# Optimization experiments

Measured on AMD Instinct MI355X. Metric: run time of the kernel, lower is better.

The kernel has to match this reference:

```python
import jax, jax.numpy as jnp
import numpy as np

NEG_SLOPE = 0.2
BN_EPS = 1e-5


def gat_conv(x, src, dst, num_nodes, W, att_src, att_dst, bias, concat):
    # x: [N, F_in]; W: [F_in, H*C]; att_src/att_dst: [H, C]
    H, C = att_src.shape
    h = (x @ W).reshape(num_nodes, H, C)                 # [N, H, C]
    a_src = jnp.einsum('nhc,hc->nh', h, att_src)          # [N, H]
    a_dst = jnp.einsum('nhc,hc->nh', h, att_dst)          # [N, H]
    e = a_src[src] + a_dst[dst]                           # [E, H]
    e = jax.nn.leaky_relu(e, NEG_SLOPE)
    # segment softmax over edges sharing the same destination node
    m = jax.ops.segment_max(e, dst, num_segments=num_nodes)   # [N, H]
    ex = jnp.exp(e - m[dst])
    denom = jax.ops.segment_sum(ex, dst, num_segments=num_nodes)  # [N, H]
    alpha = ex / (denom[dst] + 1e-16)                     # [E, H]
    msg = h[src] * alpha[:, :, None]                      # [E, H, C]
    out = jax.ops.segment_sum(msg, dst, num_segments=num_nodes)   # [N, H, C]
    if concat:
        return out.reshape(num_nodes, H * C) + bias
    return out.mean(axis=1) + bias


def batch_norm(x, gamma, beta):
    mu = x.mean(axis=0)
    var = x.var(axis=0)
    return (x - mu) * jax.lax.rsqrt(var + BN_EPS) * gamma + beta


def setup_inputs() -> dict:
    key = jax.random.key(0)
    ks = jax.random.split(key, 16)
    N, E, F_in, C, H, NC = 50000, 800000, 128, 16, 8, 2
    s = lambda k, shape, fan: jax.random.normal(k, shape, jnp.float32) * (1.0 / np.sqrt(fan))
    inp = {
        'x': jax.random.normal(ks[0], (N, F_in), jnp.float32),
        'edge_index': jax.random.randint(ks[1], (2, E), 0, N, jnp.int32),
        'W0': s(ks[2], (F_in, H * C), F_in),
        'att_src0': s(ks[3], (H, C), C),
        'att_dst0': s(ks[4], (H, C), C),
        'b0': jnp.zeros((H * C,), jnp.float32),
        'gamma0': jnp.ones((H * C,), jnp.float32),
        'beta0': jnp.zeros((H * C,), jnp.float32),
        'W1': s(ks[5], (H * C, H * C), H * C),
        'att_src1': s(ks[6], (H, C), C),
        'att_dst1': s(ks[7], (H, C), C),
        'b1': jnp.zeros((C,), jnp.float32),
        'gamma1': jnp.ones((C,), jnp.float32),
        'beta1': jnp.zeros((C,), jnp.float32),
        'Wc': s(ks[8], (C, NC), C),
        'bc': jnp.zeros((NC,), jnp.float32),
    }
    return inp


def reference(x, edge_index, W0, att_src0, att_dst0, b0, gamma0, beta0,
              W1, att_src1, att_dst1, b1, gamma1, beta1, Wc, bc):
    N = x.shape[0]
    loop = jnp.arange(N, dtype=edge_index.dtype)
    src = jnp.concatenate([edge_index[0], loop])  # add self-loops (PyG default)
    dst = jnp.concatenate([edge_index[1], loop])
    # layer 0: concat heads -> [N, H*C]
    h = gat_conv(x, src, dst, N, W0, att_src0, att_dst0, b0, concat=True)
    h = batch_norm(h, gamma0, beta0)
    h = jax.nn.elu(h)
    # layer 1: average heads -> [N, C]
    h = gat_conv(h, src, dst, N, W1, att_src1, att_dst1, b1, concat=False)
    h = batch_norm(h, gamma1, beta1)
    logits = h @ Wc + bc
    return logits
```

## Files before the change

kernel.cpp:

```cpp
#include <hip/hip_runtime.h>
#include <math.h>

#define NEG_SLOPE 0.2f
#define BN_EPS 1e-5f

typedef __attribute__((ext_vector_type(8))) short bf16x8;
typedef __attribute__((ext_vector_type(4))) float f32x4;
typedef __attribute__((ext_vector_type(8))) unsigned short us8;


__device__ __forceinline__ void edge_sd(const int* __restrict__ ei, int E, int eid, int& s, int& d) {
    if (eid < E) { s = ei[eid]; d = ei[E + eid]; }
    else         { s = d = eid - E; }
}

__device__ __forceinline__ float lrelu(float v) { return v > 0.f ? v : NEG_SLOPE * v; }

__device__ __forceinline__ unsigned short f2bf(float f) {
    unsigned u = __float_as_uint(f);
    u += 0x7fffu + ((u >> 16) & 1u);
    return (unsigned short)(u >> 16);
}

__global__ void wtrans_kernel(const float* __restrict__ W0, const float* __restrict__ as0,
                              const float* __restrict__ ad0,
                              const float* __restrict__ W1, const float* __restrict__ as1,
                              const float* __restrict__ ad1,
                              unsigned short* __restrict__ Wt0, unsigned short* __restrict__ Wt1) {
    int idx = blockIdx.x * 256 + threadIdx.x;
    const float *W, *as_, *ad_;
    unsigned short* Wt;
    int i;
    if (idx < 18432) { W = W0; as_ = as0; ad_ = ad0; Wt = Wt0; i = idx; }
    else             { W = W1; as_ = as1; ad_ = ad1; Wt = Wt1; i = idx - 18432; }
    if (i < 16384) {
        int k = i >> 7, n = i & 127;
        Wt[(n >> 4) * 2048 + (n & 15) * 128 + k] = f2bf(W[k * 128 + n]);
    } else {
        int j = i - 16384;
        int k = j >> 4, hh = j & 15;
        int h = hh & 7;
        const float* av = (hh < 8) ? as_ : ad_;
        float s = 0.f;
#pragma unroll
        for (int c = 0; c < 16; c++) s += W[k * 128 + h * 16 + c] * av[h * 16 + c];
        Wt[8 * 2048 + hh * 128 + k] = f2bf(s);
    }
}

__global__ __launch_bounds__(256) void gemm_att_kernel(const float* __restrict__ X,
                                                       const unsigned short* __restrict__ Wt,
                                                       unsigned short* __restrict__ Hbf,
                                                       float* __restrict__ a_src,
                                                       float* __restrict__ a_dst,
                                                       const float* __restrict__ bnmu,
                                                       const float* __restrict__ bnrs,
                                                       const float* __restrict__ gamma,
                                                       const float* __restrict__ beta,
                                                       int Nrows) {
    __shared__ unsigned short xs[64 * 136];
    int bm = blockIdx.x * 64;
    int tid = threadIdx.x;

    for (int i = tid; i < 64 * 16; i += 256) {
        int row = i >> 4;
        int c8 = (i & 15) * 8;
        int grow = bm + row;
        float v[8];
        if (grow < Nrows) {
            float4 v0 = *(const float4*)(X + (size_t)grow * 128 + c8);
            float4 v1 = *(const float4*)(X + (size_t)grow * 128 + c8 + 4);
            v[0] = v0.x; v[1] = v0.y; v[2] = v0.z; v[3] = v0.w;
            v[4] = v1.x; v[5] = v1.y; v[6] = v1.z; v[7] = v1.w;
        } else {
#pragma unroll
            for (int j = 0; j < 8; j++) v[j] = 0.f;
        }
        if (bnmu != nullptr) {
#pragma unroll
            for (int j = 0; j < 8; j++) {
                int c = c8 + j;
                float t = (v[j] - bnmu[c]) * bnrs[c] * gamma[c] + beta[c];
                v[j] = t > 0.f ? t : expm1f(t);
            }
        }
        us8 p;
#pragma unroll
        for (int j = 0; j < 8; j++) p[j] = f2bf(v[j]);
        *(us8*)(xs + row * 136 + c8) = p;
    }
    __syncthreads();

    int w = tid >> 6, lane = tid & 63;
    int m16 = lane & 15;
    int quad = lane >> 4;

    f32x4 acc[9];
#pragma unroll
    for (int c = 0; c < 9; c++) acc[c] = (f32x4){0.f, 0.f, 0.f, 0.f};

    const unsigned short* xrow = xs + (w * 16 + m16) * 136 + quad * 8;
#pragma unroll
    for (int ks = 0; ks < 4; ks++) {
        bf16x8 a = *(const bf16x8*)(xrow + ks * 32);
#pragma unroll
        for (int c = 0; c < 9; c++) {
            bf16x8 b = *(const bf16x8*)(Wt + c * 2048 + m16 * 128 + ks * 32 + quad * 8);
            acc[c] = __builtin_amdgcn_mfma_f32_16x16x32_bf16(a, b, acc[c], 0, 0, 0);
        }
    }

    int rowb = bm + w * 16 + quad * 4;
#pragma unroll
    for (int c = 0; c < 8; c++) {
#pragma unroll
        for (int r = 0; r < 4; r++) {
            int row = rowb + r;
            if (row < Nrows)
                Hbf[(size_t)row * 128 + c * 16 + m16] = f2bf(acc[c][r]);
        }
    }
#pragma unroll
    for (int r = 0; r < 4; r++) {
        int row = rowb + r;
        if (row < Nrows) {
            if (m16 < 8) a_src[row * 8 + m16] = acc[8][r];
            else         a_dst[row * 8 + (m16 - 8)] = acc[8][r];
        }
    }
}

__global__ void hist_kernel(const int* __restrict__ ei, int E, int Etot,
                            int* __restrict__ counts, int* __restrict__ rank) {
    int eid = blockIdx.x * 256 + threadIdx.x;
    if (eid >= Etot) return;
    int s, d;
    edge_sd(ei, E, eid, s, d);
    rank[eid] = atomicAdd(&counts[d], 1);
}

__global__ __launch_bounds__(256) void chunksum_kernel(const int* __restrict__ counts,
                                                       int* __restrict__ csum, int N) {
    __shared__ int red[256];
    int base = blockIdx.x * 1024;
    int s = 0;
    for (int i = threadIdx.x; i < 1024; i += 256) {
        int idx = base + i;
        s += (idx < N) ? counts[idx] : 0;
    }
    red[threadIdx.x] = s;
    __syncthreads();
#pragma unroll
    for (int st = 128; st > 0; st >>= 1) {
        if (threadIdx.x < st) red[threadIdx.x] += red[threadIdx.x + st];
        __syncthreads();
    }
    if (threadIdx.x == 0) csum[blockIdx.x] = red[0];
}

__global__ void chunkscan_kernel(int* __restrict__ csum, int nchunk) {
    int lane = threadIdx.x;
    int v = (lane < nchunk) ? csum[lane] : 0;
    int incl = v;
#pragma unroll
    for (int off = 1; off < 64; off <<= 1) {
        int t = __shfl_up(incl, off);
        if (lane >= off) incl += t;
    }
    if (lane < nchunk) csum[lane] = incl - v;
}

__global__ __launch_bounds__(1024) void scanfinal_kernel(const int* __restrict__ counts,
                                                         const int* __restrict__ csum,
                                                         int* __restrict__ rowptr, int N) {
    __shared__ int wsum[16], woff_s[16];
    int tid = threadIdx.x, lane = tid & 63, wid = tid >> 6;
    int idx = blockIdx.x * 1024 + tid;
    int v = (idx < N) ? counts[idx] : 0;
    int incl = v;
#pragma unroll
    for (int off = 1; off < 64; off <<= 1) {
        int t = __shfl_up(incl, off);
        if (lane >= off) incl += t;
    }
    if (lane == 63) wsum[wid] = incl;
    __syncthreads();
    if (wid == 0 && lane < 16) {
        int w = wsum[lane], iw = w;
#pragma unroll
        for (int off = 1; off < 16; off <<= 1) {
            int t = __shfl_up(iw, off);
            if (lane >= off) iw += t;
        }
        woff_s[lane] = iw - w;
    }
    __syncthreads();
    if (idx < N) rowptr[idx + 1] = csum[blockIdx.x] + woff_s[wid] + incl;
    if (blockIdx.x == 0 && tid == 0) rowptr[0] = 0;
}

__global__ void scatter_kernel(const int* __restrict__ ei, int E, int Etot,
                               const int* __restrict__ rowptr, const int* __restrict__ rank,
                               unsigned short* __restrict__ ssrc) {
    int eid = blockIdx.x * 256 + threadIdx.x;
    if (eid >= Etot) return;
    int s, d;
    edge_sd(ei, E, eid, s, d);
    ssrc[rowptr[d] + rank[eid]] = (unsigned short)s;
}

template <bool MEAN>
__global__ __launch_bounds__(256) void agg_kernel(const int* __restrict__ rowptr,
                                                  const unsigned short* __restrict__ ssrc,
                                                  const float* __restrict__ a_src,
                                                  const float* __restrict__ a_dst,
                                                  const unsigned short* __restrict__ Hbf,
                                                  float* __restrict__ outbuf, int N) {
    int wid = threadIdx.x >> 6;
    int dst = blockIdx.x * 4 + wid;
    if (dst >= N) return;
    int lane = threadIdx.x & 63;
    int j  = lane >> 3;
    int hj = lane & 7;
    int hf = lane >> 3;
    int f  = lane * 2;
    int start = rowptr[dst], end = rowptr[dst + 1];
    float adst = a_dst[dst * 8 + hj];

    float acc0 = 0.f, acc1 = 0.f, denl = 0.f;
    for (int base = start; base < end; base += 8) {
        int i = base + j;
        int s = (i < end) ? (int)ssrc[i] : -1;
        float w = 0.f;
        if (s >= 0) w = __expf(lrelu(a_src[s * 8 + hj] + adst));
        denl += w;

        int   sA[8];
        float wA[8];
        unsigned uA[8];
#pragma unroll
        for (int j2 = 0; j2 < 8; j2++) {
            sA[j2] = __shfl(s, j2 * 8);
            wA[j2] = __shfl(w, j2 * 8 + hf);
        }
#pragma unroll
        for (int j2 = 0; j2 < 8; j2++)
            uA[j2] = (sA[j2] >= 0) ? *(const unsigned*)(Hbf + (size_t)sA[j2] * 128 + f) : 0u;
#pragma unroll
        for (int j2 = 0; j2 < 8; j2++) {
            acc0 += wA[j2] * __uint_as_float(uA[j2] << 16);
            acc1 += wA[j2] * __uint_as_float(uA[j2] & 0xffff0000u);
        }
    }
#pragma unroll
    for (int off = 8; off < 64; off <<= 1) denl += __shfl_xor(denl, off);
    float den = __shfl(denl, hf);
    float inv = 1.f / (den + 1e-16f);
    if (!MEAN) {
        *(float2*)(outbuf + (size_t)dst * 128 + f) = make_float2(acc0 * inv, acc1 * inv);
    } else {
        float r0 = acc0 * inv, r1 = acc1 * inv;
#pragma unroll
        for (int off = 8; off < 64; off <<= 1) {
            r0 += __shfl_xor(r0, off);
            r1 += __shfl_xor(r1, off);
        }
        if (lane < 8)
            *(float2*)(outbuf + (size_t)dst * 16 + lane * 2) =
                make_float2(r0 * 0.125f, r1 * 0.125f);
    }
}

template <int C>
__global__ __launch_bounds__(256) void stats_part_kernel(const float* __restrict__ X, int Nrows,
                                                         float* __restrict__ partial,
                                                         int rows_per_block) {
    constexpr int GSZ = 256 / C;
    __shared__ float ls[256], lq[256];
    int c = threadIdx.x % C;
    int g = threadIdx.x / C;
    long base = (long)blockIdx.x * rows_per_block;
    long endr = base + rows_per_block;
    if (endr > Nrows) endr = Nrows;
    float s = 0.f, q = 0.f;
    for (long r = base + g; r < endr; r += GSZ) {
        float v = X[r * C + c];
        s += v;
        q += v * v;
    }
    ls[threadIdx.x] = s;
    lq[threadIdx.x] = q;
    __syncthreads();
#pragma unroll
    for (int st = GSZ / 2; st > 0; st >>= 1) {
        if (g < st) {
            ls[threadIdx.x] += ls[threadIdx.x + st * C];
            lq[threadIdx.x] += lq[threadIdx.x + st * C];
        }
        __syncthreads();
    }
    if (g == 0) {
        partial[(size_t)blockIdx.x * (2 * C) + c] = ls[c];
        partial[(size_t)blockIdx.x * (2 * C) + C + c] = lq[c];
    }
}

template <int C>
__global__ __launch_bounds__(1024) void stats_final_kernel(const float* __restrict__ partial,
                                                           int nblk, float invN,
                                                           float* __restrict__ mu,
                                                           float* __restrict__ rsig) {
    constexpr int G = 1024 / C;
    __shared__ float ls[1024], lq[1024];
    int c = threadIdx.x % C;
    int g = threadIdx.x / C;
    float s = 0.f, q = 0.f;
    for (int b = g; b < nblk; b += G) {
        s += partial[(size_t)b * (2 * C) + c];
        q += partial[(size_t)b * (2 * C) + C + c];
    }
    ls[threadIdx.x] = s;
    lq[threadIdx.x] = q;
    __syncthreads();
#pragma unroll
    for (int st = G / 2; st > 0; st >>= 1) {
        if (g < st) {
            ls[threadIdx.x] += ls[threadIdx.x + st * C];
            lq[threadIdx.x] += lq[threadIdx.x + st * C];
        }
        __syncthreads();
    }
    if (g == 0) {
        float m_ = ls[c] * invN;
        float v = lq[c] * invN - m_ * m_;
        mu[c] = m_;
        rsig[c] = rsqrtf(v + BN_EPS);
    }
}

__global__ void final_kernel(const float* __restrict__ out1,
                             const float* __restrict__ mu, const float* __restrict__ rsig,
                             const float* __restrict__ gamma, const float* __restrict__ beta,
                             const float* __restrict__ Wc, const float* __restrict__ bc,
                             float* __restrict__ out, int N) {
    int n = blockIdx.x * 256 + threadIdx.x;
    if (n >= N) return;
    float l0 = bc[0], l1 = bc[1];
#pragma unroll
    for (int c = 0; c < 16; c++) {
        float v = (out1[(size_t)n * 16 + c] - mu[c]) * rsig[c] * gamma[c] + beta[c];
        l0 += v * Wc[c * 2 + 0];
        l1 += v * Wc[c * 2 + 1];
    }
    out[(size_t)n * 2 + 0] = l0;
    out[(size_t)n * 2 + 1] = l1;
}

extern "C" void kernel_launch(void* const* d_in, const int* in_sizes, int n_in,
                              void* d_out, int out_size, void* d_ws, size_t ws_size,
                              hipStream_t stream) {
    const float* x   = (const float*)d_in[0];
    const int*   ei  = (const int*)d_in[1];
    const float* W0  = (const float*)d_in[2];
    const float* as0 = (const float*)d_in[3];
    const float* ad0 = (const float*)d_in[4];
    const float* g0  = (const float*)d_in[6];
    const float* be0 = (const float*)d_in[7];
    const float* W1  = (const float*)d_in[8];
    const float* as1 = (const float*)d_in[9];
    const float* ad1 = (const float*)d_in[10];
    const float* g1  = (const float*)d_in[12];
    const float* be1 = (const float*)d_in[13];
    const float* Wc  = (const float*)d_in[14];
    const float* bc  = (const float*)d_in[15];
    float* out = (float*)d_out;

    int N = in_sizes[0] / 128;
    int E = in_sizes[1] / 2;
    int Etot = E + N;

    char* ws = (char*)d_ws;
    size_t off = 0;
    auto walloc = [&](size_t bytes) -> void* {
        void* p = ws + off;
        off += (bytes + 255) & ~(size_t)255;
        return p;
    };
    float*          B       = (float*)walloc((size_t)N * 128 * 4);
    unsigned short* Hbf     = (unsigned short*)walloc((size_t)N * 128 * 2);
    unsigned short* Wt0     = (unsigned short*)walloc(144 * 128 * 2);
    unsigned short* Wt1     = (unsigned short*)walloc(144 * 128 * 2);
    float*          a_src   = (float*)walloc((size_t)N * 8 * 4);
    float*          a_dst   = (float*)walloc((size_t)N * 8 * 4);
    float*          out1    = (float*)walloc((size_t)N * 16 * 4);
    int*            counts  = (int*)walloc((size_t)N * 4);
    int*            rowptr  = (int*)walloc((size_t)(N + 1) * 4);
    int*            rank    = (int*)walloc((size_t)Etot * 4);
    int*            csum    = (int*)walloc(64 * 4);
    unsigned short* ssrc    = (unsigned short*)walloc((size_t)Etot * 2);
    float*          partial = (float*)walloc((size_t)256 * 256 * 4);
    float*          stats   = (float*)walloc(2 * 128 * 4);
    float* mu = stats, * rsig = stats + 128;

    dim3 b256(256);
    int gN64    = (N + 63) / 64;
    int gE      = (Etot + 255) / 256;
    int gAgg    = (N + 3) / 4;
    int nchunk  = (N + 1023) / 1024;
    const int SBLK = 256;
    int rpb = (N + SBLK - 1) / SBLK;

    hipMemsetAsync(counts, 0, (size_t)N * 4, stream);
    hist_kernel<<<gE, b256, 0, stream>>>(ei, E, Etot, counts, rank);
    chunksum_kernel<<<nchunk, b256, 0, stream>>>(counts, csum, N);
    chunkscan_kernel<<<1, 64, 0, stream>>>(csum, nchunk);
    scanfinal_kernel<<<nchunk, 1024, 0, stream>>>(counts, csum, rowptr, N);
    scatter_kernel<<<gE, b256, 0, stream>>>(ei, E, Etot, rowptr, rank, ssrc);

    wtrans_kernel<<<144, b256, 0, stream>>>(W0, as0, ad0, W1, as1, ad1, Wt0, Wt1);

    gemm_att_kernel<<<gN64, b256, 0, stream>>>(x, Wt0, Hbf, a_src, a_dst,
                                               nullptr, nullptr, nullptr, nullptr, N);
    agg_kernel<false><<<gAgg, b256, 0, stream>>>(rowptr, ssrc, a_src, a_dst, Hbf, B, N);
    stats_part_kernel<128><<<SBLK, b256, 0, stream>>>(B, N, partial, rpb);
    stats_final_kernel<128><<<1, 1024, 0, stream>>>(partial, SBLK, 1.0f / N, mu, rsig);

    gemm_att_kernel<<<gN64, b256, 0, stream>>>(B, Wt1, Hbf, a_src, a_dst,
                                               mu, rsig, g0, be0, N);
    agg_kernel<true><<<gAgg, b256, 0, stream>>>(rowptr, ssrc, a_src, a_dst, Hbf, out1, N);
    stats_part_kernel<16><<<SBLK, b256, 0, stream>>>(out1, N, partial, rpb);
    stats_final_kernel<16><<<1, 1024, 0, stream>>>(partial, SBLK, 1.0f / N, mu, rsig);
    final_kernel<<<(N + 255) / 256, b256, 0, stream>>>(out1, mu, rsig, g1, be1, Wc, bc, out, N);
}
```

Before: 383.2 us.

## Make GEMM kernel persistent with LDS-staged weights and direct register A-fragments

The projection GEMM becomes a persistent kernel with a fixed grid of 256 blocks. Each block loads the 9 bf16 weight tiles into padded LDS once, and each wave loops over 16-row tiles. It loads X rows straight into registers as MFMA A fragments instead of staging them through shared memory, and the BN affine transform is precomputed as scale/shift in LDS. This removes repeated global weight reads per block and the X LDS round trip, at the cost of less parallelism per tile (only 1024 waves) and possibly less latency hiding on the global X loads.

```diff
diff --git a/kernel.cpp b/kernel.cpp
--- a/kernel.cpp
+++ b/kernel.cpp
@@ -6,7 +6,6 @@
 
 typedef __attribute__((ext_vector_type(8))) short bf16x8;
 typedef __attribute__((ext_vector_type(4))) float f32x4;
-typedef __attribute__((ext_vector_type(8))) unsigned short us8;
 
 
 __device__ __forceinline__ void edge_sd(const int* __restrict__ ei, int E, int eid, int& s, int& d) {
@@ -48,84 +47,108 @@
     }
 }
 
-__global__ __launch_bounds__(256) void gemm_att_kernel(const float* __restrict__ X,
-                                                       const unsigned short* __restrict__ Wt,
-                                                       unsigned short* __restrict__ Hbf,
-                                                       float* __restrict__ a_src,
-                                                       float* __restrict__ a_dst,
-                                                       const float* __restrict__ bnmu,
-                                                       const float* __restrict__ bnrs,
-                                                       const float* __restrict__ gamma,
-                                                       const float* __restrict__ beta,
-                                                       int Nrows) {
-    __shared__ unsigned short xs[64 * 136];
-    int bm = blockIdx.x * 64;
+#define WCOLSTRIDE 132
+#define WTILESZ (16 * WCOLSTRIDE)
+__global__ __launch_bounds__(256, 4) void gemm_att_kernel(const float* __restrict__ X,
+                                                          const unsigned short* __restrict__ Wt,
+                                                          unsigned short* __restrict__ Hbf,
+                                                          float* __restrict__ a_src,
+                                                          float* __restrict__ a_dst,
+                                                          const float* __restrict__ bnmu,
+                                                          const float* __restrict__ bnrs,
+                                                          const float* __restrict__ gamma,
+                                                          const float* __restrict__ beta,
+                                                          int Nrows) {
+    __shared__ unsigned short wl[9 * WTILESZ];
+    __shared__ float ss[256];
     int tid = threadIdx.x;
 
-    for (int i = tid; i < 64 * 16; i += 256) {
-        int row = i >> 4;
-        int c8 = (i & 15) * 8;
-        int grow = bm + row;
-        float v[8];
-        if (grow < Nrows) {
-            float4 v0 = *(const float4*)(X + (size_t)grow * 128 + c8);
-            float4 v1 = *(const float4*)(X + (size_t)grow * 128 + c8 + 4);
-            v[0] = v0.x; v[1] = v0.y; v[2] = v0.z; v[3] = v0.w;
-            v[4] = v1.x; v[5] = v1.y; v[6] = v1.z; v[7] = v1.w;
-        } else {
-#pragma unroll
-            for (int j = 0; j < 8; j++) v[j] = 0.f;
-        }
+    if (tid < 128) {
+        float sc = 1.f, sh = 0.f;
         if (bnmu != nullptr) {
-#pragma unroll
-            for (int j = 0; j < 8; j++) {
-                int c = c8 + j;
-                float t = (v[j] - bnmu[c]) * bnrs[c] * gamma[c] + beta[c];
-                v[j] = t > 0.f ? t : expm1f(t);
-            }
-        }
-        us8 p;
-#pragma unroll
-        for (int j = 0; j < 8; j++) p[j] = f2bf(v[j]);
-        *(us8*)(xs + row * 136 + c8) = p;
+            float rg = bnrs[tid] * gamma[tid];
+            sc = rg;
+            sh = beta[tid] - bnmu[tid] * rg;
+        }
+        ss[tid] = sc;
+        ss[128 + tid] = sh;
+    }
+    for (int i = tid; i < 9 * 16 * 16; i += 256) {
+        int c = i >> 8, rem = i & 255, col = rem >> 4, k8 = rem & 15;
+        uint4 v = *(const uint4*)(Wt + c * 2048 + col * 128 + k8 * 8);
+        *(uint4*)(wl + c * WTILESZ + col * WCOLSTRIDE + k8 * 8) = v;
     }
     __syncthreads();
 
     int w = tid >> 6, lane = tid & 63;
     int m16 = lane & 15;
     int quad = lane >> 4;
-
-    f32x4 acc[9];
-#pragma unroll
-    for (int c = 0; c < 9; c++) acc[c] = (f32x4){0.f, 0.f, 0.f, 0.f};
-
-    const unsigned short* xrow = xs + (w * 16 + m16) * 136 + quad * 8;
-#pragma unroll
-    for (int ks = 0; ks < 4; ks++) {
-        bf16x8 a = *(const bf16x8*)(xrow + ks * 32);
-#pragma unroll
-        for (int c = 0; c < 9; c++) {
-            bf16x8 b = *(const bf16x8*)(Wt + c * 2048 + m16 * 128 + ks * 32 + quad * 8);
-            acc[c] = __builtin_amdgcn_mfma_f32_16x16x32_bf16(a, b, acc[c], 0, 0, 0);
-        }
-    }
-
-    int rowb = bm + w * 16 + quad * 4;
-#pragma unroll
-    for (int c = 0; c < 8; c++) {
+    int gw = blockIdx.x * 4 + w;
+    int nw = gridDim.x * 4;
+    int ntiles = (Nrows + 15) / 16;
+    bool dobn = (bnmu != nullptr);
+    const float* scp = ss + quad * 8;
+    const float* shp = ss + 128 + quad * 8;
+
+    for (int t = gw; t < ntiles; t += nw) {
+        int rl = t * 16 + m16;
+        if (rl >= Nrows) rl = Nrows - 1;
+        const float* Xr = X + (size_t)rl * 128 + quad * 8;
+
+        float4 u[8];
+#pragma unroll
+        for (int ks = 0; ks < 4; ks++) {
+            u[2 * ks]     = *(const float4*)(Xr + ks * 32);
+            u[2 * ks + 1] = *(const float4*)(Xr + ks * 32 + 4);
+        }
+        bf16x8 afr[4];
+#pragma unroll
+        for (int ks = 0; ks < 4; ks++) {
+            float vv[8] = {u[2 * ks].x, u[2 * ks].y, u[2 * ks].z, u[2 * ks].w,
+                           u[2 * ks + 1].x, u[2 * ks + 1].y, u[2 * ks + 1].z, u[2 * ks + 1].w};
+            if (dobn) {
+#pragma unroll
+                for (int j = 0; j < 8; j++) {
+                    float tv = vv[j] * scp[ks * 32 + j] + shp[ks * 32 + j];
+                    vv[j] = tv > 0.f ? tv : expm1f(tv);
+                }
+            }
+            union { bf16x8 b; unsigned short s[8]; } pk;
+#pragma unroll
+            for (int j = 0; j < 8; j++) pk.s[j] = f2bf(vv[j]);
+            afr[ks] = pk.b;
+        }
+
+        f32x4 acc[9];
+#pragma unroll
+        for (int c = 0; c < 9; c++) acc[c] = (f32x4){0.f, 0.f, 0.f, 0.f};
+        const unsigned short* wb = wl + m16 * WCOLSTRIDE + quad * 8;
+#pragma unroll
+        for (int ks = 0; ks < 4; ks++) {
+#pragma unroll
+            for (int c = 0; c < 9; c++) {
+                bf16x8 b = *(const bf16x8*)(wb + c * WTILESZ + ks * 32);
+                acc[c] = __builtin_amdgcn_mfma_f32_16x16x32_bf16(afr[ks], b, acc[c], 0, 0, 0);
+            }
+        }
+
+        int rowb = t * 16 + quad * 4;
+#pragma unroll
+        for (int c = 0; c < 8; c++) {
+#pragma unroll
+            for (int r = 0; r < 4; r++) {
+                int row = rowb + r;
+                if (row < Nrows)
+                    Hbf[(size_t)row * 128 + c * 16 + m16] = f2bf(acc[c][r]);
+            }
+        }
 #pragma unroll
         for (int r = 0; r < 4; r++) {
             int row = rowb + r;
-            if (row < Nrows)
-                Hbf[(size_t)row * 128 + c * 16 + m16] = f2bf(acc[c][r]);
-        }
-    }
-#pragma unroll
-    for (int r = 0; r < 4; r++) {
-        int row = rowb + r;
-        if (row < Nrows) {
-            if (m16 < 8) a_src[row * 8 + m16] = acc[8][r];
-            else         a_dst[row * 8 + (m16 - 8)] = acc[8][r];
+            if (row < Nrows) {
+                if (m16 < 8) a_src[row * 8 + m16] = acc[8][r];
+                else         a_dst[row * 8 + (m16 - 8)] = acc[8][r];
+            }
         }
     }
 }
@@ -403,11 +426,11 @@
     float* mu = stats, * rsig = stats + 128;
 
     dim3 b256(256);
-    int gN64    = (N + 63) / 64;
     int gE      = (Etot + 255) / 256;
     int gAgg    = (N + 3) / 4;
     int nchunk  = (N + 1023) / 1024;
     const int SBLK = 256;
+    const int GEMMBLK = 256;
     int rpb = (N + SBLK - 1) / SBLK;
 
     hipMemsetAsync(counts, 0, (size_t)N * 4, stream);
@@ -419,14 +442,14 @@
 
     wtrans_kernel<<<144, b256, 0, stream>>>(W0, as0, ad0, W1, as1, ad1, Wt0, Wt1);
 
-    gemm_att_kernel<<<gN64, b256, 0, stream>>>(x, Wt0, Hbf, a_src, a_dst,
-                                               nullptr, nullptr, nullptr, nullptr, N);
+    gemm_att_kernel<<<GEMMBLK, b256, 0, stream>>>(x, Wt0, Hbf, a_src, a_dst,
+                                                  nullptr, nullptr, nullptr, nullptr, N);
     agg_kernel<false><<<gAgg, b256, 0, stream>>>(rowptr, ssrc, a_src, a_dst, Hbf, B, N);
     stats_part_kernel<128><<<SBLK, b256, 0, stream>>>(B, N, partial, rpb);
     stats_final_kernel<128><<<1, 1024, 0, stream>>>(partial, SBLK, 1.0f / N, mu, rsig);
 
-    gemm_att_kernel<<<gN64, b256, 0, stream>>>(B, Wt1, Hbf, a_src, a_dst,
-                                               mu, rsig, g0, be0, N);
+    gemm_att_kernel<<<GEMMBLK, b256, 0, stream>>>(B, Wt1, Hbf, a_src, a_dst,
+                                                  mu, rsig, g0, be0, N);
     agg_kernel<true><<<gAgg, b256, 0, stream>>>(rowptr, ssrc, a_src, a_dst, Hbf, out1, N);
     stats_part_kernel<16><<<SBLK, b256, 0, stream>>>(out1, N, partial, rpb);
     stats_final_kernel<16><<<1, 1024, 0, stream>>>(partial, SBLK, 1.0f / N, mu, rsig);
```

New measurement: 364.0 us. 5.0% less time.
